# Performance work log

Hardware: AMD Instinct MI355X
Metric: run time of the kernel (lower is better)

Reference implementation:

```python
import jax, jax.numpy as jnp
import numpy as np

HIDDEN = 1024
NUM_HEADS = 16
HEAD_DIM = HIDDEN // NUM_HEADS  # 64


def setup_inputs() -> dict:
    key = jax.random.key(0)
    ks = jax.random.split(key, 10)
    B, S = 2, 2048
    X = jax.random.normal(ks[0], (B, S, HIDDEN), dtype=jnp.float32)
    attention_mask = jnp.ones((B, 1, 1, S), dtype=jnp.int32)
    s = 1.0 / np.sqrt(HIDDEN)
    Wq = jax.random.uniform(ks[1], (HIDDEN, NUM_HEADS * HEAD_DIM), jnp.float32, -s, s)
    bq = jnp.zeros((NUM_HEADS * HEAD_DIM,), jnp.float32)
    Wk = jax.random.uniform(ks[2], (HIDDEN, HEAD_DIM), jnp.float32, -s, s)
    bk = jnp.zeros((HEAD_DIM,), jnp.float32)
    Wv = jax.random.uniform(ks[3], (HIDDEN, HEAD_DIM), jnp.float32, -s, s)
    bv = jnp.zeros((HEAD_DIM,), jnp.float32)
    Wo = jax.random.uniform(ks[4], (HIDDEN, HIDDEN), jnp.float32, -s, s)
    bo = jnp.zeros((HIDDEN,), jnp.float32)
    return {"X": X, "Wq": Wq, "bq": bq, "Wk": Wk, "bk": bk,
            "Wv": Wv, "bv": bv, "Wo": Wo, "bo": bo,
            "attention_mask": attention_mask}


def reference(X, Wq, bq, Wk, bk, Wv, bv, Wo, bo, attention_mask):
    B, S, _ = X.shape
    H, D = NUM_HEADS, HEAD_DIM
    # projections
    q = (X @ Wq + bq).reshape(B, S, H, D).transpose(0, 2, 1, 3)  # [B,H,S,D]
    k = (X @ Wk + bk)  # [B,S,D] single KV head
    v = (X @ Wv + bv)  # [B,S,D]
    # scores: broadcast single KV head across all query heads (repeat_interleave equiv)
    scores = jnp.einsum("bhsd,btd->bhst", q, k) / np.sqrt(D)  # [B,H,S,S]
    scores = jnp.where(attention_mask == 0, -jnp.inf, scores)
    weights = jax.nn.softmax(scores, axis=-1)
    # dropout in eval mode -> identity
    out = jnp.einsum("bhst,btd->bhsd", weights, v)  # [B,H,S,D]
    out = out.transpose(0, 2, 1, 3).reshape(B, S, H * D)
    return out @ Wo + bo
```

## Files before the change

kernel.cpp:

```cpp
#include <hip/hip_runtime.h>
#include <hip/hip_bf16.h>
#include <stdint.h>


#define DI __device__ __forceinline__

typedef unsigned short u16;
typedef __attribute__((ext_vector_type(8))) __bf16 bf16x8;
typedef __attribute__((ext_vector_type(4))) float f32x4;
typedef __attribute__((ext_vector_type(4))) float float4v;
typedef __attribute__((ext_vector_type(4))) u16 u16x4;

DI u16 f2bf(float f) {
  union { float f; unsigned int u; } v; v.f = f;
  unsigned int u = v.u;
  return (u16)((u + 0x7FFFu + ((u >> 16) & 1u)) >> 16);
}

DI void async16(void* lds, const void* g) {
  __builtin_amdgcn_global_load_lds(
      (const __attribute__((address_space(1))) unsigned int*)g,
      (__attribute__((address_space(3))) unsigned int*)lds, 16, 0, 0);
}

DI void stage_rows(const u16* __restrict__ g, long gstride, char* lds,
                   int nchunks, int tid) {
  int w = tid >> 6, lane = tid & 63;
  for (int base = w * 64; base < nchunks; base += 256) {
    int chunk = base + lane;
    int row = chunk >> 3;
    int cc = (chunk & 7) ^ (row & 7);
    async16(lds + base * 16, g + (long)row * gstride + cc * 8);
  }
}

DI bf16x8 read_frag(const char* lds, int row, int kchunk) {
  return *(const bf16x8*)(lds + row * 128 + ((kchunk ^ (row & 7)) << 4));
}

DI f32x4 MFMA(bf16x8 a, bf16x8 b, f32x4 c) {
  return __builtin_amdgcn_mfma_f32_16x16x32_bf16(a, b, c, 0, 0, 0);
}


__global__ void cvt_f32_bf16_kernel(const float* __restrict__ src,
                                    u16* __restrict__ dst, int n4) {
  int i = blockIdx.x * blockDim.x + threadIdx.x;
  if (i >= n4) return;
  float4v v = *(const float4v*)(src + (long)i * 4);
  u16x4 o;
  o[0] = f2bf(v[0]); o[1] = f2bf(v[1]); o[2] = f2bf(v[2]); o[3] = f2bf(v[3]);
  *(u16x4*)(dst + (long)i * 4) = o;
}

__global__ void transpose_f32_bf16(const float* __restrict__ src,
                                   u16* __restrict__ dst, int K, int N) {
  __shared__ float t[32][33];
  int nt = blockIdx.x % (N >> 5), kt = blockIdx.x / (N >> 5);
  int c = threadIdx.x & 31, r0 = threadIdx.x >> 5;
#pragma unroll
  for (int i = 0; i < 4; i++) {
    int r = r0 + i * 8;
    t[r][c] = src[(long)(kt * 32 + r) * N + nt * 32 + c];
  }
  __syncthreads();
#pragma unroll
  for (int i = 0; i < 4; i++) {
    int r = r0 + i * 8;
    dst[(long)(nt * 32 + r) * K + kt * 32 + c] = f2bf(t[c][r]);
  }
}


template <int EPI>
__global__ __launch_bounds__(256, 2) void gemm_bf16(
    const u16* __restrict__ A, const u16* __restrict__ Bt, int N, int K,
    u16* __restrict__ Qb, u16* __restrict__ Kb, u16* __restrict__ Vt,
    const float* __restrict__ bq, const float* __restrict__ bk,
    const float* __restrict__ bv, float* __restrict__ Cout,
    const float* __restrict__ bo) {
  __shared__ __attribute__((aligned(16))) char lds[2][32768];
  const int tid = threadIdx.x, lane = tid & 63, w = tid >> 6;
  const int nTiles = N >> 7;
  const int mt = blockIdx.x / nTiles, nt = blockIdx.x % nTiles;
  const int m0 = mt << 7, n0 = nt << 7;
  const int wm = w >> 1, wn = w & 1;
  const int lrow = lane & 15, lk = lane >> 4;

  f32x4 acc[4][4] = {};

  stage_rows(A + (long)m0 * K, K, lds[0], 1024, tid);
  stage_rows(Bt + (long)n0 * K, K, lds[0] + 16384, 1024, tid);
  __syncthreads();

  const int NT = K >> 6;
  int cur = 0;
  for (int t = 0; t < NT; t++) {
    if (t + 1 < NT) {
      stage_rows(A + (long)m0 * K + (t + 1) * 64, K, lds[cur ^ 1], 1024, tid);
      stage_rows(Bt + (long)n0 * K + (t + 1) * 64, K, lds[cur ^ 1] + 16384,
                 1024, tid);
    }
    const char* La = lds[cur];
    const char* Lb = lds[cur] + 16384;
#pragma unroll
    for (int kk = 0; kk < 2; kk++) {
      bf16x8 af[4], bfr[4];
#pragma unroll
      for (int i = 0; i < 4; i++) {
        af[i] = read_frag(La, wm * 64 + i * 16 + lrow, kk * 4 + lk);
        bfr[i] = read_frag(Lb, wn * 64 + i * 16 + lrow, kk * 4 + lk);
      }
#pragma unroll
      for (int mf = 0; mf < 4; mf++)
#pragma unroll
        for (int nf = 0; nf < 4; nf++)
          acc[mf][nf] = MFMA(af[mf], bfr[nf], acc[mf][nf]);
    }
    __syncthreads();
    cur ^= 1;
  }

#pragma unroll
  for (int mf = 0; mf < 4; mf++) {
#pragma unroll
    for (int nf = 0; nf < 4; nf++) {
      int col = n0 + wn * 64 + nf * 16 + lrow;
#pragma unroll
      for (int r = 0; r < 4; r++) {
        int row = m0 + wm * 64 + mf * 16 + lk * 4 + r;
        float x = acc[mf][nf][r];
        if (EPI == 0) {
          if (col < 1024) {
            Qb[(long)row * 1024 + col] = f2bf((x + bq[col]) * 0.125f);
          } else if (col < 1088) {
            int d = col - 1024;
            Kb[(long)row * 64 + d] = f2bf(x + bk[d]);
          } else {
            int d = col - 1088;
            int b = row >> 11, s = row & 2047;
            Vt[((long)(b * 64 + d)) * 2048 + s] = f2bf(x + bv[d]);
          }
        } else {
          Cout[(long)row * 1024 + col] = x + bo[col];
        }
      }
    }
  }
}

__global__ __launch_bounds__(256, 2) void attn_kernel(
    const u16* __restrict__ Qb, const u16* __restrict__ Kb,
    const u16* __restrict__ Vt, u16* __restrict__ attnb) {
  __shared__ __attribute__((aligned(16))) char ldsQ[16384];
  __shared__ __attribute__((aligned(16))) char ldsK[2][8192];
  __shared__ __attribute__((aligned(16))) char ldsV[2][8192];
  __shared__ __attribute__((aligned(16))) char ldsP[16384];

  const int tid = threadIdx.x, lane = tid & 63, w = tid >> 6;
  const int lrow = lane & 15, lk = lane >> 4;
  const int qt = blockIdx.x & 15;
  const int bh = blockIdx.x >> 4;
  const int b = bh >> 4, h = bh & 15;
  const int q0 = qt << 7;

  const u16* Qg = Qb + ((long)(b * 2048 + q0)) * 1024 + h * 64;
  const u16* Kg = Kb + ((long)b * 2048) * 64;
  const u16* Vg = Vt + ((long)b * 64) * 2048;

  stage_rows(Qg, 1024, ldsQ, 1024, tid);
  stage_rows(Kg, 64, ldsK[0], 512, tid);
  stage_rows(Vg, 2048, ldsV[0], 512, tid);
  __syncthreads();

  bf16x8 qa[2][2];
#pragma unroll
  for (int qf = 0; qf < 2; qf++)
#pragma unroll
    for (int kk = 0; kk < 2; kk++)
      qa[qf][kk] = read_frag(ldsQ, w * 32 + qf * 16 + lrow, kk * 4 + lk);

  f32x4 acc[2][4] = {};
  float m_run[2][4], l_run[2][4];
#pragma unroll
  for (int qf = 0; qf < 2; qf++)
#pragma unroll
    for (int r = 0; r < 4; r++) { m_run[qf][r] = -1e30f; l_run[qf][r] = 0.f; }

  int cur = 0;
  for (int t = 0; t < 32; t++) {
    if (t + 1 < 32) {
      stage_rows(Kg + (t + 1) * 64 * 64, 64, ldsK[cur ^ 1], 512, tid);
      stage_rows(Vg + (t + 1) * 64, 2048, ldsV[cur ^ 1], 512, tid);
    }
    f32x4 s[2][4] = {};
#pragma unroll
    for (int kk = 0; kk < 2; kk++) {
      bf16x8 kb[4];
#pragma unroll
      for (int kf = 0; kf < 4; kf++)
        kb[kf] = read_frag(ldsK[cur], kf * 16 + lrow, kk * 4 + lk);
#pragma unroll
      for (int qf = 0; qf < 2; qf++)
#pragma unroll
        for (int kf = 0; kf < 4; kf++)
          s[qf][kf] = MFMA(qa[qf][kk], kb[kf], s[qf][kf]);
    }
#pragma unroll
    for (int qf = 0; qf < 2; qf++) {
#pragma unroll
      for (int r = 0; r < 4; r++) {
        float mx = fmaxf(fmaxf(s[qf][0][r], s[qf][1][r]),
                         fmaxf(s[qf][2][r], s[qf][3][r]));
#pragma unroll
        for (int msk = 1; msk < 16; msk <<= 1)
          mx = fmaxf(mx, __shfl_xor(mx, msk));
        float mnew = fmaxf(m_run[qf][r], mx);
        float alpha = __expf(m_run[qf][r] - mnew);
        m_run[qf][r] = mnew;
        int q = w * 32 + qf * 16 + lk * 4 + r;
        char* prow = ldsP + q * 128;
        int sw = (q & 7) << 4;
        float ps = 0.f;
#pragma unroll
        for (int kf = 0; kf < 4; kf++) {
          float p = __expf(s[qf][kf][r] - mnew);
          ps += p;
          int col = kf * 16 + lrow;
          *(u16*)(prow + (((col >> 3) << 4) ^ sw) + (col & 7) * 2) = f2bf(p);
        }
#pragma unroll
        for (int msk = 1; msk < 16; msk <<= 1)
          ps += __shfl_xor(ps, msk);
        l_run[qf][r] = l_run[qf][r] * alpha + ps;
#pragma unroll
        for (int df = 0; df < 4; df++) acc[qf][df][r] *= alpha;
      }
    }
#pragma unroll
    for (int kk = 0; kk < 2; kk++) {
      bf16x8 pa[2], vb[4];
#pragma unroll
      for (int qf = 0; qf < 2; qf++)
        pa[qf] = read_frag(ldsP, w * 32 + qf * 16 + lrow, kk * 4 + lk);
#pragma unroll
      for (int df = 0; df < 4; df++)
        vb[df] = read_frag(ldsV[cur], df * 16 + lrow, kk * 4 + lk);
#pragma unroll
      for (int qf = 0; qf < 2; qf++)
#pragma unroll
        for (int df = 0; df < 4; df++)
          acc[qf][df] = MFMA(pa[qf], vb[df], acc[qf][df]);
    }
    __syncthreads();
    cur ^= 1;
  }

#pragma unroll
  for (int qf = 0; qf < 2; qf++)
#pragma unroll
    for (int df = 0; df < 4; df++)
#pragma unroll
      for (int r = 0; r < 4; r++) {
        int qrow = q0 + w * 32 + qf * 16 + lk * 4 + r;
        int col = h * 64 + df * 16 + lrow;
        float o = acc[qf][df][r] / l_run[qf][r];
        attnb[((long)(b * 2048 + qrow)) * 1024 + col] = f2bf(o);
      }
}


extern "C" void kernel_launch(void* const* d_in, const int* in_sizes, int n_in,
                              void* d_out, int out_size, void* d_ws,
                              size_t ws_size, hipStream_t stream) {
  const float* X  = (const float*)d_in[0];
  const float* Wq = (const float*)d_in[1];
  const float* bq = (const float*)d_in[2];
  const float* Wk = (const float*)d_in[3];
  const float* bk = (const float*)d_in[4];
  const float* Wv = (const float*)d_in[5];
  const float* bv = (const float*)d_in[6];
  const float* Wo = (const float*)d_in[7];
  const float* bo = (const float*)d_in[8];
  float* out = (float*)d_out;

  char* ws = (char*)d_ws;
  u16* Xbf   = (u16*)(ws);
  u16* WqkvT = (u16*)(ws + 8388608);
  u16* WoT   = (u16*)(ws + 10747904);
  u16* Qb    = (u16*)(ws + 12845056);
  u16* Kb    = (u16*)(ws + 21233664);
  u16* Vt    = (u16*)(ws + 21757952);
  u16* attnb = (u16*)(ws + 22282240);

  cvt_f32_bf16_kernel<<<4096, 256, 0, stream>>>(X, Xbf, 1048576);
  transpose_f32_bf16<<<1024, 256, 0, stream>>>(Wq, WqkvT, 1024, 1024);
  transpose_f32_bf16<<<64, 256, 0, stream>>>(Wk, WqkvT + 1024 * 1024, 1024, 64);
  transpose_f32_bf16<<<64, 256, 0, stream>>>(Wv, WqkvT + 1088 * 1024, 1024, 64);
  transpose_f32_bf16<<<1024, 256, 0, stream>>>(Wo, WoT, 1024, 1024);

  gemm_bf16<0><<<288, 256, 0, stream>>>(Xbf, WqkvT, 1152, 1024, Qb, Kb, Vt,
                                        bq, bk, bv, nullptr, nullptr);
  attn_kernel<<<512, 256, 0, stream>>>(Qb, Kb, Vt, attnb);
  gemm_bf16<1><<<256, 256, 0, stream>>>(attnb, WoT, 1024, 1024, nullptr,
                                        nullptr, nullptr, nullptr, nullptr,
                                        nullptr, out, bo);
}
```

Before: 251.2 us.

## Shrink GEMM and attention tiles, add lazy rescale and MFMA row-sum

```diff
diff --git a/kernel.cpp b/kernel.cpp
--- a/kernel.cpp
+++ b/kernel.cpp
@@ -72,49 +72,52 @@
 }
 
 
-template <int EPI>
-__global__ __launch_bounds__(256, 2) void gemm_bf16(
+template <int EPI, int BN>
+__global__ __launch_bounds__(256, 3) void gemm_bf16(
     const u16* __restrict__ A, const u16* __restrict__ Bt, int N, int K,
     u16* __restrict__ Qb, u16* __restrict__ Kb, u16* __restrict__ Vt,
     const float* __restrict__ bq, const float* __restrict__ bk,
     const float* __restrict__ bv, float* __restrict__ Cout,
     const float* __restrict__ bo) {
-  __shared__ __attribute__((aligned(16))) char lds[2][32768];
+  constexpr int NF = BN / 32;
+  constexpr int ACH = 1024, BCH = BN * 8;
+  __shared__ __attribute__((aligned(16))) char lds[2][16384 + BN * 128];
   const int tid = threadIdx.x, lane = tid & 63, w = tid >> 6;
-  const int nTiles = N >> 7;
+  const int nTiles = N / BN;
   const int mt = blockIdx.x / nTiles, nt = blockIdx.x % nTiles;
-  const int m0 = mt << 7, n0 = nt << 7;
+  const int m0 = mt << 7, n0 = nt * BN;
   const int wm = w >> 1, wn = w & 1;
   const int lrow = lane & 15, lk = lane >> 4;
 
-  f32x4 acc[4][4] = {};
-
-  stage_rows(A + (long)m0 * K, K, lds[0], 1024, tid);
-  stage_rows(Bt + (long)n0 * K, K, lds[0] + 16384, 1024, tid);
+  f32x4 acc[4][NF] = {};
+
+  stage_rows(A + (long)m0 * K, K, lds[0], ACH, tid);
+  stage_rows(Bt + (long)n0 * K, K, lds[0] + 16384, BCH, tid);
   __syncthreads();
 
   const int NT = K >> 6;
   int cur = 0;
   for (int t = 0; t < NT; t++) {
     if (t + 1 < NT) {
-      stage_rows(A + (long)m0 * K + (t + 1) * 64, K, lds[cur ^ 1], 1024, tid);
+      stage_rows(A + (long)m0 * K + (t + 1) * 64, K, lds[cur ^ 1], ACH, tid);
       stage_rows(Bt + (long)n0 * K + (t + 1) * 64, K, lds[cur ^ 1] + 16384,
-                 1024, tid);
+                 BCH, tid);
     }
     const char* La = lds[cur];
     const char* Lb = lds[cur] + 16384;
 #pragma unroll
     for (int kk = 0; kk < 2; kk++) {
-      bf16x8 af[4], bfr[4];
-#pragma unroll
-      for (int i = 0; i < 4; i++) {
+      bf16x8 af[4], bfr[NF];
+#pragma unroll
+      for (int i = 0; i < 4; i++)
         af[i] = read_frag(La, wm * 64 + i * 16 + lrow, kk * 4 + lk);
-        bfr[i] = read_frag(Lb, wn * 64 + i * 16 + lrow, kk * 4 + lk);
-      }
+#pragma unroll
+      for (int i = 0; i < NF; i++)
+        bfr[i] = read_frag(Lb, wn * (BN / 2) + i * 16 + lrow, kk * 4 + lk);
 #pragma unroll
       for (int mf = 0; mf < 4; mf++)
 #pragma unroll
-        for (int nf = 0; nf < 4; nf++)
+        for (int nf = 0; nf < NF; nf++)
           acc[mf][nf] = MFMA(af[mf], bfr[nf], acc[mf][nf]);
     }
     __syncthreads();
@@ -124,8 +127,8 @@
 #pragma unroll
   for (int mf = 0; mf < 4; mf++) {
 #pragma unroll
-    for (int nf = 0; nf < 4; nf++) {
-      int col = n0 + wn * 64 + nf * 16 + lrow;
+    for (int nf = 0; nf < NF; nf++) {
+      int col = n0 + wn * (BN / 2) + nf * 16 + lrow;
 #pragma unroll
       for (int r = 0; r < 4; r++) {
         int row = m0 + wm * 64 + mf * 16 + lk * 4 + r;
@@ -149,43 +152,42 @@
   }
 }
 
-__global__ __launch_bounds__(256, 2) void attn_kernel(
+__global__ __launch_bounds__(256, 4) void attn_kernel(
     const u16* __restrict__ Qb, const u16* __restrict__ Kb,
     const u16* __restrict__ Vt, u16* __restrict__ attnb) {
-  __shared__ __attribute__((aligned(16))) char ldsQ[16384];
+  __shared__ __attribute__((aligned(16))) char ldsQP[8192];
   __shared__ __attribute__((aligned(16))) char ldsK[2][8192];
   __shared__ __attribute__((aligned(16))) char ldsV[2][8192];
-  __shared__ __attribute__((aligned(16))) char ldsP[16384];
 
   const int tid = threadIdx.x, lane = tid & 63, w = tid >> 6;
   const int lrow = lane & 15, lk = lane >> 4;
-  const int qt = blockIdx.x & 15;
-  const int bh = blockIdx.x >> 4;
+  const int qt = blockIdx.x & 31;
+  const int bh = blockIdx.x >> 5;
   const int b = bh >> 4, h = bh & 15;
-  const int q0 = qt << 7;
+  const int q0 = qt << 6;
 
   const u16* Qg = Qb + ((long)(b * 2048 + q0)) * 1024 + h * 64;
   const u16* Kg = Kb + ((long)b * 2048) * 64;
   const u16* Vg = Vt + ((long)b * 64) * 2048;
 
-  stage_rows(Qg, 1024, ldsQ, 1024, tid);
+  stage_rows(Qg, 1024, ldsQP, 512, tid);
   stage_rows(Kg, 64, ldsK[0], 512, tid);
   stage_rows(Vg, 2048, ldsV[0], 512, tid);
   __syncthreads();
 
-  bf16x8 qa[2][2];
-#pragma unroll
-  for (int qf = 0; qf < 2; qf++)
-#pragma unroll
-    for (int kk = 0; kk < 2; kk++)
-      qa[qf][kk] = read_frag(ldsQ, w * 32 + qf * 16 + lrow, kk * 4 + lk);
-
-  f32x4 acc[2][4] = {};
-  float m_run[2][4], l_run[2][4];
-#pragma unroll
-  for (int qf = 0; qf < 2; qf++)
-#pragma unroll
-    for (int r = 0; r < 4; r++) { m_run[qf][r] = -1e30f; l_run[qf][r] = 0.f; }
+  bf16x8 qa[2];
+#pragma unroll
+  for (int kk = 0; kk < 2; kk++)
+    qa[kk] = read_frag(ldsQP, w * 16 + lrow, kk * 4 + lk);
+
+  f32x4 acc[4] = {};
+  float m_run[4], l_run[4];
+#pragma unroll
+  for (int r = 0; r < 4; r++) { m_run[r] = -1e30f; l_run[r] = 0.f; }
+
+  bf16x8 vones;
+#pragma unroll
+  for (int i = 0; i < 8; i++) vones[i] = (__bf16)1.0f;
 
   int cur = 0;
   for (int t = 0; t < 32; t++) {
@@ -193,7 +195,8 @@
       stage_rows(Kg + (t + 1) * 64 * 64, 64, ldsK[cur ^ 1], 512, tid);
       stage_rows(Vg + (t + 1) * 64, 2048, ldsV[cur ^ 1], 512, tid);
     }
-    f32x4 s[2][4] = {};
+    f32x4 s[4] = {};
+    __builtin_amdgcn_s_setprio(1);
 #pragma unroll
     for (int kk = 0; kk < 2; kk++) {
       bf16x8 kb[4];
@@ -201,72 +204,63 @@
       for (int kf = 0; kf < 4; kf++)
         kb[kf] = read_frag(ldsK[cur], kf * 16 + lrow, kk * 4 + lk);
 #pragma unroll
-      for (int qf = 0; qf < 2; qf++)
-#pragma unroll
-        for (int kf = 0; kf < 4; kf++)
-          s[qf][kf] = MFMA(qa[qf][kk], kb[kf], s[qf][kf]);
-    }
-#pragma unroll
-    for (int qf = 0; qf < 2; qf++) {
-#pragma unroll
-      for (int r = 0; r < 4; r++) {
-        float mx = fmaxf(fmaxf(s[qf][0][r], s[qf][1][r]),
-                         fmaxf(s[qf][2][r], s[qf][3][r]));
-#pragma unroll
-        for (int msk = 1; msk < 16; msk <<= 1)
-          mx = fmaxf(mx, __shfl_xor(mx, msk));
-        float mnew = fmaxf(m_run[qf][r], mx);
-        float alpha = __expf(m_run[qf][r] - mnew);
-        m_run[qf][r] = mnew;
-        int q = w * 32 + qf * 16 + lk * 4 + r;
-        char* prow = ldsP + q * 128;
-        int sw = (q & 7) << 4;
-        float ps = 0.f;
-#pragma unroll
-        for (int kf = 0; kf < 4; kf++) {
-          float p = __expf(s[qf][kf][r] - mnew);
-          ps += p;
-          int col = kf * 16 + lrow;
-          *(u16*)(prow + (((col >> 3) << 4) ^ sw) + (col & 7) * 2) = f2bf(p);
-        }
-#pragma unroll
-        for (int msk = 1; msk < 16; msk <<= 1)
-          ps += __shfl_xor(ps, msk);
-        l_run[qf][r] = l_run[qf][r] * alpha + ps;
-#pragma unroll
-        for (int df = 0; df < 4; df++) acc[qf][df][r] *= alpha;
+      for (int kf = 0; kf < 4; kf++)
+        s[kf] = MFMA(qa[kk], kb[kf], s[kf]);
+    }
+    __builtin_amdgcn_s_setprio(0);
+#pragma unroll
+    for (int r = 0; r < 4; r++) {
+      float mx = fmaxf(fmaxf(s[0][r], s[1][r]), fmaxf(s[2][r], s[3][r]));
+#pragma unroll
+      for (int msk = 1; msk < 16; msk <<= 1)
+        mx = fmaxf(mx, __shfl_xor(mx, msk));
+      if (mx > m_run[r] + 8.f) {
+        float alpha = __expf(m_run[r] - mx);
+        m_run[r] = mx;
+        l_run[r] *= alpha;
+#pragma unroll
+        for (int df = 0; df < 4; df++) acc[df][r] *= alpha;
       }
-    }
+      int q = w * 16 + lk * 4 + r;
+      char* prow = ldsQP + q * 128;
+      int sw = (q & 7) << 4;
+#pragma unroll
+      for (int kf = 0; kf < 4; kf++) {
+        float p = __expf(s[kf][r] - m_run[r]);
+        int col = kf * 16 + lrow;
+        *(u16*)(prow + (((col >> 3) << 4) ^ sw) + (col & 7) * 2) = f2bf(p);
+      }
+    }
+    f32x4 lsum = {};
+    __builtin_amdgcn_s_setprio(1);
 #pragma unroll
     for (int kk = 0; kk < 2; kk++) {
-      bf16x8 pa[2], vb[4];
-#pragma unroll
-      for (int qf = 0; qf < 2; qf++)
-        pa[qf] = read_frag(ldsP, w * 32 + qf * 16 + lrow, kk * 4 + lk);
+      bf16x8 pa = read_frag(ldsQP, w * 16 + lrow, kk * 4 + lk);
+      bf16x8 vb[4];
 #pragma unroll
       for (int df = 0; df < 4; df++)
         vb[df] = read_frag(ldsV[cur], df * 16 + lrow, kk * 4 + lk);
 #pragma unroll
-      for (int qf = 0; qf < 2; qf++)
-#pragma unroll
-        for (int df = 0; df < 4; df++)
-          acc[qf][df] = MFMA(pa[qf], vb[df], acc[qf][df]);
-    }
+      for (int df = 0; df < 4; df++)
+        acc[df] = MFMA(pa, vb[df], acc[df]);
+      lsum = MFMA(pa, vones, lsum);
+    }
+    __builtin_amdgcn_s_setprio(0);
+#pragma unroll
+    for (int r = 0; r < 4; r++) l_run[r] += lsum[r];
     __syncthreads();
     cur ^= 1;
   }
 
 #pragma unroll
-  for (int qf = 0; qf < 2; qf++)
-#pragma unroll
-    for (int df = 0; df < 4; df++)
-#pragma unroll
-      for (int r = 0; r < 4; r++) {
-        int qrow = q0 + w * 32 + qf * 16 + lk * 4 + r;
-        int col = h * 64 + df * 16 + lrow;
-        float o = acc[qf][df][r] / l_run[qf][r];
-        attnb[((long)(b * 2048 + qrow)) * 1024 + col] = f2bf(o);
-      }
+  for (int df = 0; df < 4; df++)
+#pragma unroll
+    for (int r = 0; r < 4; r++) {
+      int qrow = q0 + w * 16 + lk * 4 + r;
+      int col = h * 64 + df * 16 + lrow;
+      float o = acc[df][r] / l_run[r];
+      attnb[((long)(b * 2048 + qrow)) * 1024 + col] = f2bf(o);
+    }
 }
 
 
@@ -299,10 +293,10 @@
   transpose_f32_bf16<<<64, 256, 0, stream>>>(Wv, WqkvT + 1088 * 1024, 1024, 64);
   transpose_f32_bf16<<<1024, 256, 0, stream>>>(Wo, WoT, 1024, 1024);
 
-  gemm_bf16<0><<<288, 256, 0, stream>>>(Xbf, WqkvT, 1152, 1024, Qb, Kb, Vt,
-                                        bq, bk, bv, nullptr, nullptr);
-  attn_kernel<<<512, 256, 0, stream>>>(Qb, Kb, Vt, attnb);
-  gemm_bf16<1><<<256, 256, 0, stream>>>(attnb, WoT, 1024, 1024, nullptr,
-                                        nullptr, nullptr, nullptr, nullptr,
-                                        nullptr, out, bo);
-}
+  gemm_bf16<0, 64><<<576, 256, 0, stream>>>(Xbf, WqkvT, 1152, 1024, Qb, Kb, Vt,
+                                            bq, bk, bv, nullptr, nullptr);
+  attn_kernel<<<1024, 256, 0, stream>>>(Qb, Kb, Vt, attnb);
+  gemm_bf16<1, 64><<<512, 256, 0, stream>>>(attnb, WoT, 1024, 1024, nullptr,
+                                            nullptr, nullptr, nullptr, nullptr,
+                                            nullptr, out, bo);
+}
```

New measurement: 223.6 us. -11.0%, faster.
